# Kernel tuning notes

Measured on AMD Instinct MI355X. Metric: run time of the kernel, lower is better.

## Reference

```python
import jax, jax.numpy as jnp
import numpy as np

EMBED_DIM = 1024
HEAD_DIM = 64
B, T = 4, 4096


def setup_inputs() -> dict:
    key = jax.random.key(0)
    kx, kq, kk, kv = jax.random.split(key, 4)
    x = jax.random.normal(kx, (B, T, EMBED_DIM), dtype=jnp.float32)
    # nn.Linear weights, stored transposed as (in, out) for x @ W
    s = 1.0 / np.sqrt(EMBED_DIM)
    Wq = jax.random.normal(kq, (EMBED_DIM, HEAD_DIM), dtype=jnp.float32) * s
    Wk = jax.random.normal(kk, (EMBED_DIM, HEAD_DIM), dtype=jnp.float32) * s
    Wv = jax.random.normal(kv, (EMBED_DIM, HEAD_DIM), dtype=jnp.float32) * s
    return {"x": x, "Wq": Wq, "Wk": Wk, "Wv": Wv}


def reference(x, Wq, Wk, Wv):
    Bc, Tc, C = x.shape
    Q = x @ Wq  # [B, T, H]
    K = x @ Wk
    V = x @ Wv
    # NOTE: original scales by embedding_dim C, not head_dim
    scores = jnp.einsum('bqh,bkh->bqk', Q, K) / jnp.sqrt(jnp.float32(C))
    causal = jnp.tril(jnp.ones((Tc, Tc), dtype=bool))
    scores = jnp.where(causal, scores, -jnp.inf)
    attn = jax.nn.softmax(scores, axis=-1)
    return jnp.einsum('bqk,bkh->bqh', attn, V)
```

## Files before the change

kernel.cpp:

```cpp
#include <hip/hip_runtime.h>
#include <hip/hip_bf16.h>
#include <math.h>

typedef __attribute__((ext_vector_type(8))) short bf16x8;
typedef __attribute__((ext_vector_type(4))) float f32x4;

#define MFMA16 __builtin_amdgcn_mfma_f32_16x16x32_bf16

static constexpr int TSEQ = 4096;
static constexpr int EMB = 1024;
static constexpr int HD = 64;

__device__ __forceinline__ unsigned short f2bf(float f) {
    unsigned u = __builtin_bit_cast(unsigned, f);
    u += 0x7fffu + ((u >> 16) & 1u);
    return (unsigned short)(u >> 16);
}

__device__ __forceinline__ void gll16(const void* g, void* l) {
    __builtin_amdgcn_global_load_lds(
        (const __attribute__((address_space(1))) void*)g,
        (__attribute__((address_space(3))) void*)l, 16, 0, 0);
}

__global__ void prep_w(const float* __restrict__ Wq, const float* __restrict__ Wk,
                       const float* __restrict__ Wv, unsigned short* __restrict__ Wp) {
    int id = blockIdx.x * 256 + threadIdx.x;
    int wsel = id >> 16;
    int t = id & 65535;
    int k = t >> 6, n0 = t & 63;
    const float* W = (wsel == 0) ? Wq : (wsel == 1) ? Wk : Wv;
    float v = W[t];
    if (wsel == 0) v *= 0.03125f;
    int n = wsel * 64 + n0;
    Wp[(k >> 5) * 6144 + n * 32 + (k & 31)] = f2bf(v);
}

__global__ __launch_bounds__(512, 4) void proj_kernel(const float* __restrict__ X,
        const unsigned short* __restrict__ Wp, unsigned short* __restrict__ Qp,
        unsigned short* __restrict__ Kp, unsigned short* __restrict__ Vp) {
    __shared__ unsigned short wlds[2][6144];
    __shared__ unsigned short xlds[2][1024];

    const int tid = threadIdx.x;
    const int lane = tid & 63, wave = tid >> 6;
    const int col = lane & 15, quad = lane >> 4;
    const int mw = wave >> 2, nw = wave & 3;
    const int row0 = blockIdx.x * 32;

    f32x4 acc[3];
#pragma unroll
    for (int j = 0; j < 3; j++) acc[j] = (f32x4)(0.0f);

    const char* wsrc = (const char*)Wp + lane * 16;
    auto stageW = [&](int slab, int b) {
        const char* s = wsrc + (size_t)slab * 12288;
        char* d = (char*)&wlds[b][0];
        gll16(s + nw * 1024,       d + nw * 1024);
        gll16(s + (4 + nw) * 1024, d + (4 + nw) * 1024);
        gll16(s + (8 + nw) * 1024, d + (8 + nw) * 1024);
    };
    const int u = tid - 256;
    const int xrow = u >> 3, xseg = u & 7;
    const float* xsrc = X + (size_t)(row0 + xrow) * EMB + xseg * 4;
    const int xdst = (xrow >> 4) * 1024 + (xseg >> 1) * 256 + (xrow & 15) * 16 + (xseg & 1) * 8;

    float4 xg = (float4)(0.0f);
    if (mw == 1) {
        float4 v = *(const float4*)(xsrc);
        ushort4 p; p.x = f2bf(v.x); p.y = f2bf(v.y); p.z = f2bf(v.z); p.w = f2bf(v.w);
        *(ushort4*)((char*)&xlds[0][0] + xdst) = p;
        xg = *(const float4*)(xsrc + 32);
    } else {
        stageW(0, 0);
    }
    __syncthreads();

#pragma unroll 2
    for (int kc = 0; kc < 32; kc++) {
        const int b = kc & 1;
        if (mw == 0) {
            if (kc + 1 < 32) stageW(kc + 1, b ^ 1);
        } else {
            if (kc + 1 < 32) {
                float4 xn = xg;
                if (kc + 2 < 32) xn = *(const float4*)(xsrc + (kc + 2) * 32);
                ushort4 p; p.x = f2bf(xg.x); p.y = f2bf(xg.y);
                p.z = f2bf(xg.z); p.w = f2bf(xg.w);
                *(ushort4*)((char*)&xlds[b ^ 1][0] + xdst) = p;
                xg = xn;
            }
        }
        const bf16x8 A = *(const bf16x8*)((const char*)&xlds[b][0] + mw * 1024 + lane * 16);
        const char* wb = (const char*)&wlds[b][0] + col * 64 + quad * 16;
        acc[0] = MFMA16(A, *(const bf16x8*)(wb + nw * 1024),       acc[0], 0, 0, 0);
        acc[1] = MFMA16(A, *(const bf16x8*)(wb + (4 + nw) * 1024), acc[1], 0, 0, 0);
        acc[2] = MFMA16(A, *(const bf16x8*)(wb + (8 + nw) * 1024), acc[2], 0, 0, 0);
        __syncthreads();
    }

    const int tile = blockIdx.x * 2 + mw;
#pragma unroll
    for (int r = 0; r < 4; r++)
        Qp[tile * 1024 + (nw >> 1) * 512 + (quad * 4 + r) * 32 +
           ((nw & 1) * 2 + (col >> 3)) * 8 + (col & 7)] = f2bf(acc[0][r]);
#pragma unroll
    for (int r = 0; r < 4; r++)
        Kp[(tile * 2 + (nw >> 1)) * 512 + (quad * 4 + r) * 32 +
           ((nw & 1) * 2 + (col >> 3)) * 8 + (col & 7)] = f2bf(acc[1][r]);
    {
        ushort4 pk;
        pk.x = f2bf(acc[2][0]); pk.y = f2bf(acc[2][1]);
        pk.z = f2bf(acc[2][2]); pk.w = f2bf(acc[2][3]);
        *(ushort4*)&Vp[blockIdx.x * 2048 + nw * 512 + col * 32 + mw * 16 + quad * 4] = pk;
    }
}

__global__ __launch_bounds__(512, 4) void attn_kernel(const unsigned short* __restrict__ Qp,
        const unsigned short* __restrict__ Kp, const unsigned short* __restrict__ Vp,
        float* __restrict__ Out) {
    __shared__ float cmb[4][2][64][20];
    __shared__ unsigned short plds[8][2][640];
    const int lane = threadIdx.x & 63, wave = threadIdx.x >> 6;
    const int col = lane & 15, quad = lane >> 4;
    const int batch = blockIdx.x & 3;
    const int ti = 127 - (blockIdx.x >> 2);
    const int q0 = ti * 32;
    const size_t bT = (size_t)batch * TSEQ;
    const int fragoff = col * 64 + quad * 16;

    const char* QpB = (const char*)Qp;
    const char* KpB = (const char*)Kp;
    const char* VpB = (const char*)Vp;
    const int gt = (int)((bT + q0) >> 4);
    const int c0 = (int)(bT >> 5);

    bf16x8 aq[2][2];
#pragma unroll
    for (int m = 0; m < 2; m++)
#pragma unroll
        for (int h = 0; h < 2; h++)
            aq[m][h] = *(const bf16x8*)(QpB + (size_t)((gt + m) * 2 + h) * 1024 + fragoff);

    f32x4 o[2][4];
    f32x4 lsum[2];
#pragma unroll
    for (int m = 0; m < 2; m++) {
        lsum[m] = (f32x4)(0.0f);
#pragma unroll
        for (int t = 0; t < 4; t++) o[m][t] = (f32x4)(0.0f);
    }

    for (int c = wave; c <= ti; c += 8) {
        const char* kb = KpB + (size_t)(c0 + c) * 4096;
        const char* vb = VpB + (size_t)(c0 + c) * 4096;
        bf16x8 bk[2][2], bv[4];
#pragma unroll
        for (int j = 0; j < 2; j++)
#pragma unroll
            for (int h = 0; h < 2; h++)
                bk[j][h] = *(const bf16x8*)(kb + j * 2048 + h * 1024 + fragoff);
#pragma unroll
        for (int t = 0; t < 4; t++)
            bv[t] = *(const bf16x8*)(vb + t * 1024 + fragoff);

        f32x4 s[2][2];
#pragma unroll
        for (int m = 0; m < 2; m++)
#pragma unroll
            for (int j = 0; j < 2; j++) {
                f32x4 a = MFMA16(aq[m][0], bk[j][0], (f32x4)(0.0f), 0, 0, 0);
                s[m][j] = MFMA16(aq[m][1], bk[j][1], a, 0, 0, 0);
            }
        const bool diag = (c == ti);
#pragma unroll
        for (int m = 0; m < 2; m++)
#pragma unroll
            for (int j = 0; j < 2; j++)
#pragma unroll
                for (int r = 0; r < 4; r++) {
                    float v = s[m][j][r];
                    if (diag && (j * 16 + col > m * 16 + quad * 4 + r)) v = -INFINITY;
                    const float p = __expf(v);
                    lsum[m][r] += p;
                    plds[wave][m][(quad * 4 + r) * 40 + j * 16 + col] =
                        (unsigned short)(__builtin_bit_cast(unsigned, p) >> 16);
                }
        bf16x8 pa[2];
#pragma unroll
        for (int m = 0; m < 2; m++)
            pa[m] = *(const bf16x8*)(&plds[wave][m][col * 40 + quad * 8]);
#pragma unroll
        for (int m = 0; m < 2; m++)
#pragma unroll
            for (int t = 0; t < 4; t++)
                o[m][t] = MFMA16(pa[m], bv[t], o[m][t], 0, 0, 0);
    }

    auto wr = [&](int s) {
#pragma unroll
        for (int m = 0; m < 2; m++) {
#pragma unroll
            for (int t = 0; t < 4; t++)
                *(f32x4*)&cmb[s][m][lane][t * 4] = o[m][t];
            *(f32x4*)&cmb[s][m][lane][16] = lsum[m];
        }
    };
    auto rd = [&](int s) {
#pragma unroll
        for (int m = 0; m < 2; m++) {
#pragma unroll
            for (int t = 0; t < 4; t++)
                o[m][t] += *(const f32x4*)&cmb[s][m][lane][t * 4];
            lsum[m] += *(const f32x4*)&cmb[s][m][lane][16];
        }
    };
    if (wave >= 4) wr(wave - 4);
    __syncthreads();
    if (wave < 4) rd(wave);
    __syncthreads();
    if (wave == 2 || wave == 3) wr(wave);
    __syncthreads();
    if (wave < 2) rd(wave + 2);
    __syncthreads();
    if (wave == 1) wr(1);
    __syncthreads();
    if (wave == 0) {
        rd(1);
#pragma unroll
        for (int off = 1; off < 16; off <<= 1)
#pragma unroll
            for (int m = 0; m < 2; m++)
#pragma unroll
                for (int r = 0; r < 4; r++)
                    lsum[m][r] += __shfl_xor(lsum[m][r], off, 64);
#pragma unroll
        for (int m = 0; m < 2; m++)
#pragma unroll
            for (int r = 0; r < 4; r++) {
                const float inv = 1.0f / lsum[m][r];
                const size_t orow = (bT + q0 + m * 16 + quad * 4 + r) * HD;
#pragma unroll
                for (int t = 0; t < 4; t++)
                    Out[orow + t * 16 + col] = o[m][t][r] * inv;
            }
    }
}

extern "C" void kernel_launch(void* const* d_in, const int* in_sizes, int n_in,
                              void* d_out, int out_size, void* d_ws, size_t ws_size,
                              hipStream_t stream) {
    const float* x  = (const float*)d_in[0];
    const float* Wq = (const float*)d_in[1];
    const float* Wk = (const float*)d_in[2];
    const float* Wv = (const float*)d_in[3];
    float* out = (float*)d_out;

    char* w = (char*)d_ws;
    unsigned short* Wp = (unsigned short*)(w);
    unsigned short* Qp = (unsigned short*)(w + (512 << 10));
    unsigned short* Kp = (unsigned short*)(w + (512 << 10) + (2 << 20));
    unsigned short* Vp = (unsigned short*)(w + (512 << 10) + (4 << 20));

    hipLaunchKernelGGL(prep_w, dim3(768), dim3(256), 0, stream, Wq, Wk, Wv, Wp);
    hipLaunchKernelGGL(proj_kernel, dim3(512), dim3(512), 0, stream, x, Wp, Qp, Kp, Vp);
    hipLaunchKernelGGL(attn_kernel, dim3(512), dim3(512), 0, stream, Qp, Kp, Vp, out);
}
```

Before: 147.2 us.

## Enlarge projection tile to 64 rows and double K-step per stage

The projection kernel now handles 64 rows per block instead of 32, so each wave computes two M tiles and reuses each loaded weight fragment twice. Each pipeline stage stages two 32-wide K slabs, halving barrier count, and warp specialization now uses waves 0-3 for weight DMA and 4-7 for x conversion. The weight prep layout is changed to a fragment-contiguous order so LDS reads are linear per lane. The grid shrinks to 256 blocks with more LDS per block and occupancy is reduced to 2, which lowers parallelism.

After: 139.9 us. -4.9%, faster.

```diff
diff --git a/kernel.cpp b/kernel.cpp
--- a/kernel.cpp
+++ b/kernel.cpp
@@ -33,86 +33,141 @@
     float v = W[t];
     if (wsel == 0) v *= 0.03125f;
     int n = wsel * 64 + n0;
-    Wp[(k >> 5) * 6144 + n * 32 + (k & 31)] = f2bf(v);
-}
-
-__global__ __launch_bounds__(512, 4) void proj_kernel(const float* __restrict__ X,
+    Wp[(k >> 5) * 6144 + (n >> 4) * 512 + ((k >> 3) & 3) * 128 + (n & 15) * 8 + (k & 7)] = f2bf(v);
+}
+
+__global__ __launch_bounds__(512, 2) void proj_kernel(const float* __restrict__ X,
         const unsigned short* __restrict__ Wp, unsigned short* __restrict__ Qp,
         unsigned short* __restrict__ Kp, unsigned short* __restrict__ Vp) {
-    __shared__ unsigned short wlds[2][6144];
-    __shared__ unsigned short xlds[2][1024];
+    __shared__ unsigned short wlds[2][12288];
+    __shared__ unsigned short xlds[2][4096];
 
     const int tid = threadIdx.x;
     const int lane = tid & 63, wave = tid >> 6;
     const int col = lane & 15, quad = lane >> 4;
     const int mw = wave >> 2, nw = wave & 3;
-    const int row0 = blockIdx.x * 32;
-
-    f32x4 acc[3];
-#pragma unroll
-    for (int j = 0; j < 3; j++) acc[j] = (f32x4)(0.0f);
+    const int row0 = blockIdx.x * 64;
+
+    f32x4 acc[2][3];
+#pragma unroll
+    for (int i = 0; i < 2; i++)
+#pragma unroll
+        for (int j = 0; j < 3; j++) acc[i][j] = (f32x4)(0.0f);
 
     const char* wsrc = (const char*)Wp + lane * 16;
-    auto stageW = [&](int slab, int b) {
-        const char* s = wsrc + (size_t)slab * 12288;
-        char* d = (char*)&wlds[b][0];
-        gll16(s + nw * 1024,       d + nw * 1024);
-        gll16(s + (4 + nw) * 1024, d + (4 + nw) * 1024);
-        gll16(s + (8 + nw) * 1024, d + (8 + nw) * 1024);
-    };
-    const int u = tid - 256;
-    const int xrow = u >> 3, xseg = u & 7;
-    const float* xsrc = X + (size_t)(row0 + xrow) * EMB + xseg * 4;
-    const int xdst = (xrow >> 4) * 1024 + (xseg >> 1) * 256 + (xrow & 15) * 16 + (xseg & 1) * 8;
-
-    float4 xg = (float4)(0.0f);
-    if (mw == 1) {
-        float4 v = *(const float4*)(xsrc);
-        ushort4 p; p.x = f2bf(v.x); p.y = f2bf(v.y); p.z = f2bf(v.z); p.w = f2bf(v.w);
-        *(ushort4*)((char*)&xlds[0][0] + xdst) = p;
-        xg = *(const float4*)(xsrc + 32);
+    auto stageW = [&](int p, int b) {
+#pragma unroll
+        for (int u = 0; u < 2; u++) {
+            const char* s = wsrc + (size_t)(2 * p + u) * 12288;
+            char* d = (char*)&wlds[b][0] + u * 12288;
+            gll16(s + nw * 1024,       d + nw * 1024);
+            gll16(s + (4 + nw) * 1024, d + (4 + nw) * 1024);
+            gll16(s + (8 + nw) * 1024, d + (8 + nw) * 1024);
+        }
+    };
+    const int u2 = tid & 255;
+    const int xrow = u2 >> 3, q8 = u2 & 7;
+    const float* xsA = X + (size_t)(row0 + xrow) * EMB + q8 * 8;
+    const float* xsB = xsA + 32 * EMB;
+    const int xo = (q8 >> 2) * 4096 + (xrow >> 4) * 1024 + (q8 & 3) * 256 + (xrow & 15) * 16;
+
+    auto wr8 = [&](int b, int off, float4 f0, float4 f1) {
+        union { unsigned short s[8]; bf16x8 v; } r;
+        r.s[0] = f2bf(f0.x); r.s[1] = f2bf(f0.y); r.s[2] = f2bf(f0.z); r.s[3] = f2bf(f0.w);
+        r.s[4] = f2bf(f1.x); r.s[5] = f2bf(f1.y); r.s[6] = f2bf(f1.z); r.s[7] = f2bf(f1.w);
+        *(bf16x8*)((char*)&xlds[b][0] + off) = r.v;
+    };
+    auto compute = [&](int b) {
+        bf16x8 A[2][2], Wf[2][3];
+        const char* xb = (const char*)&xlds[b][0];
+        const char* wb = (const char*)&wlds[b][0];
+#pragma unroll
+        for (int u = 0; u < 2; u++) {
+#pragma unroll
+            for (int i = 0; i < 2; i++)
+                A[u][i] = *(const bf16x8*)(xb + u * 4096 + (mw * 2 + i) * 1024 + lane * 16);
+#pragma unroll
+            for (int j = 0; j < 3; j++)
+                Wf[u][j] = *(const bf16x8*)(wb + u * 12288 + (j * 4 + nw) * 1024 + lane * 16);
+        }
+#pragma unroll
+        for (int u = 0; u < 2; u++)
+#pragma unroll
+            for (int i = 0; i < 2; i++)
+#pragma unroll
+                for (int j = 0; j < 3; j++)
+                    acc[i][j] = MFMA16(A[u][i], Wf[u][j], acc[i][j], 0, 0, 0);
+    };
+
+    float4 pa0, pa1, pb0, pb1;
+    float4 qa0, qa1, qb0, qb1;
+    if (wave < 4) {
+        stageW(0, 0);
     } else {
-        stageW(0, 0);
-    }
-    __syncthreads();
-
-#pragma unroll 2
-    for (int kc = 0; kc < 32; kc++) {
-        const int b = kc & 1;
-        if (mw == 0) {
-            if (kc + 1 < 32) stageW(kc + 1, b ^ 1);
+        float4 t0 = *(const float4*)(xsA);
+        float4 t1 = *(const float4*)(xsA + 4);
+        float4 t2 = *(const float4*)(xsB);
+        float4 t3 = *(const float4*)(xsB + 4);
+        wr8(0, xo, t0, t1);
+        wr8(0, xo + 2048, t2, t3);
+        pa0 = *(const float4*)(xsA + 64);
+        pa1 = *(const float4*)(xsA + 68);
+        pb0 = *(const float4*)(xsB + 64);
+        pb1 = *(const float4*)(xsB + 68);
+    }
+    __syncthreads();
+
+    for (int kci = 0; kci < 8; kci++) {
+        const int kc0 = kci * 2;
+        if (wave >= 4) {
+            if (kc0 + 2 < 16) {
+                qa0 = *(const float4*)(xsA + (kc0 + 2) * 64);
+                qa1 = *(const float4*)(xsA + (kc0 + 2) * 64 + 4);
+                qb0 = *(const float4*)(xsB + (kc0 + 2) * 64);
+                qb1 = *(const float4*)(xsB + (kc0 + 2) * 64 + 4);
+            }
+            if (kc0 + 1 < 16) {
+                wr8(1, xo, pa0, pa1);
+                wr8(1, xo + 2048, pb0, pb1);
+            }
         } else {
-            if (kc + 1 < 32) {
-                float4 xn = xg;
-                if (kc + 2 < 32) xn = *(const float4*)(xsrc + (kc + 2) * 32);
-                ushort4 p; p.x = f2bf(xg.x); p.y = f2bf(xg.y);
-                p.z = f2bf(xg.z); p.w = f2bf(xg.w);
-                *(ushort4*)((char*)&xlds[b ^ 1][0] + xdst) = p;
-                xg = xn;
-            }
-        }
-        const bf16x8 A = *(const bf16x8*)((const char*)&xlds[b][0] + mw * 1024 + lane * 16);
-        const char* wb = (const char*)&wlds[b][0] + col * 64 + quad * 16;
-        acc[0] = MFMA16(A, *(const bf16x8*)(wb + nw * 1024),       acc[0], 0, 0, 0);
-        acc[1] = MFMA16(A, *(const bf16x8*)(wb + (4 + nw) * 1024), acc[1], 0, 0, 0);
-        acc[2] = MFMA16(A, *(const bf16x8*)(wb + (8 + nw) * 1024), acc[2], 0, 0, 0);
+            if (kc0 + 1 < 16) stageW(kc0 + 1, 1);
+        }
+        compute(0);
         __syncthreads();
-    }
-
-    const int tile = blockIdx.x * 2 + mw;
-#pragma unroll
-    for (int r = 0; r < 4; r++)
-        Qp[tile * 1024 + (nw >> 1) * 512 + (quad * 4 + r) * 32 +
-           ((nw & 1) * 2 + (col >> 3)) * 8 + (col & 7)] = f2bf(acc[0][r]);
-#pragma unroll
-    for (int r = 0; r < 4; r++)
-        Kp[(tile * 2 + (nw >> 1)) * 512 + (quad * 4 + r) * 32 +
-           ((nw & 1) * 2 + (col >> 3)) * 8 + (col & 7)] = f2bf(acc[1][r]);
-    {
+        if (wave >= 4) {
+            if (kc0 + 3 < 16) {
+                pa0 = *(const float4*)(xsA + (kc0 + 3) * 64);
+                pa1 = *(const float4*)(xsA + (kc0 + 3) * 64 + 4);
+                pb0 = *(const float4*)(xsB + (kc0 + 3) * 64);
+                pb1 = *(const float4*)(xsB + (kc0 + 3) * 64 + 4);
+            }
+            if (kc0 + 2 < 16) {
+                wr8(0, xo, qa0, qa1);
+                wr8(0, xo + 2048, qb0, qb1);
+            }
+        } else {
+            if (kc0 + 2 < 16) stageW(kc0 + 2, 0);
+        }
+        compute(1);
+        __syncthreads();
+    }
+
+#pragma unroll
+    for (int i = 0; i < 2; i++) {
+        const int t = blockIdx.x * 4 + mw * 2 + i;
+#pragma unroll
+        for (int r = 0; r < 4; r++)
+            Qp[t * 1024 + (nw >> 1) * 512 + (quad * 4 + r) * 32 +
+               ((nw & 1) * 2 + (col >> 3)) * 8 + (col & 7)] = f2bf(acc[i][0][r]);
+#pragma unroll
+        for (int r = 0; r < 4; r++)
+            Kp[(t * 2 + (nw >> 1)) * 512 + (quad * 4 + r) * 32 +
+               ((nw & 1) * 2 + (col >> 3)) * 8 + (col & 7)] = f2bf(acc[i][1][r]);
         ushort4 pk;
-        pk.x = f2bf(acc[2][0]); pk.y = f2bf(acc[2][1]);
-        pk.z = f2bf(acc[2][2]); pk.w = f2bf(acc[2][3]);
-        *(ushort4*)&Vp[blockIdx.x * 2048 + nw * 512 + col * 32 + mw * 16 + quad * 4] = pk;
+        pk.x = f2bf(acc[i][2][0]); pk.y = f2bf(acc[i][2][1]);
+        pk.z = f2bf(acc[i][2][2]); pk.w = f2bf(acc[i][2][3]);
+        *(ushort4*)&Vp[(t >> 1) * 2048 + nw * 512 + col * 32 + (t & 1) * 16 + quad * 4] = pk;
     }
 }
 
@@ -263,6 +318,6 @@
     unsigned short* Vp = (unsigned short*)(w + (512 << 10) + (4 << 20));
 
     hipLaunchKernelGGL(prep_w, dim3(768), dim3(256), 0, stream, Wq, Wk, Wv, Wp);
-    hipLaunchKernelGGL(proj_kernel, dim3(512), dim3(512), 0, stream, x, Wp, Qp, Kp, Vp);
+    hipLaunchKernelGGL(proj_kernel, dim3(256), dim3(512), 0, stream, x, Wp, Qp, Kp, Vp);
     hipLaunchKernelGGL(attn_kernel, dim3(512), dim3(512), 0, stream, Qp, Kp, Vp, out);
 }
```

## Double K-chunk per stage in projection kernel with MFMA-friendly weight layout

Applied to the files above, without the earlier changes.

The projection kernel now processes 64 K-elements per pipeline stage instead of 32, halving the number of barriers and loop iterations. Staging duties are split by wave: waves 0-3 load weights and waves 4-7 load and convert X, with 8-element vectorized LDS writes. The packed weight layout is reordered so each lane reads a contiguous 16-byte fragment, avoiding strided LDS reads. LDS usage doubles, which may reduce occupancy.

After: 138.4 us. 6.0% less time.

```diff
diff --git a/kernel.cpp b/kernel.cpp
--- a/kernel.cpp
+++ b/kernel.cpp
@@ -33,14 +33,14 @@
     float v = W[t];
     if (wsel == 0) v *= 0.03125f;
     int n = wsel * 64 + n0;
-    Wp[(k >> 5) * 6144 + n * 32 + (k & 31)] = f2bf(v);
+    Wp[(k >> 5) * 6144 + (n >> 4) * 512 + ((k >> 3) & 3) * 128 + (n & 15) * 8 + (k & 7)] = f2bf(v);
 }
 
 __global__ __launch_bounds__(512, 4) void proj_kernel(const float* __restrict__ X,
         const unsigned short* __restrict__ Wp, unsigned short* __restrict__ Qp,
         unsigned short* __restrict__ Kp, unsigned short* __restrict__ Vp) {
-    __shared__ unsigned short wlds[2][6144];
-    __shared__ unsigned short xlds[2][1024];
+    __shared__ unsigned short wlds[2][12288];
+    __shared__ unsigned short xlds[2][2048];
 
     const int tid = threadIdx.x;
     const int lane = tid & 63, wave = tid >> 6;
@@ -53,49 +53,80 @@
     for (int j = 0; j < 3; j++) acc[j] = (f32x4)(0.0f);
 
     const char* wsrc = (const char*)Wp + lane * 16;
-    auto stageW = [&](int slab, int b) {
-        const char* s = wsrc + (size_t)slab * 12288;
-        char* d = (char*)&wlds[b][0];
-        gll16(s + nw * 1024,       d + nw * 1024);
-        gll16(s + (4 + nw) * 1024, d + (4 + nw) * 1024);
-        gll16(s + (8 + nw) * 1024, d + (8 + nw) * 1024);
-    };
-    const int u = tid - 256;
-    const int xrow = u >> 3, xseg = u & 7;
-    const float* xsrc = X + (size_t)(row0 + xrow) * EMB + xseg * 4;
-    const int xdst = (xrow >> 4) * 1024 + (xseg >> 1) * 256 + (xrow & 15) * 16 + (xseg & 1) * 8;
-
-    float4 xg = (float4)(0.0f);
-    if (mw == 1) {
-        float4 v = *(const float4*)(xsrc);
-        ushort4 p; p.x = f2bf(v.x); p.y = f2bf(v.y); p.z = f2bf(v.z); p.w = f2bf(v.w);
-        *(ushort4*)((char*)&xlds[0][0] + xdst) = p;
-        xg = *(const float4*)(xsrc + 32);
+    auto stageW = [&](int p, int b) {
+#pragma unroll
+        for (int u = 0; u < 2; u++) {
+            const char* s = wsrc + (size_t)(2 * p + u) * 12288;
+            char* d = (char*)&wlds[b][0] + u * 12288;
+            gll16(s + nw * 1024,       d + nw * 1024);
+            gll16(s + (4 + nw) * 1024, d + (4 + nw) * 1024);
+            gll16(s + (8 + nw) * 1024, d + (8 + nw) * 1024);
+        }
+    };
+    const int u2 = tid & 255;
+    const int xrow = u2 >> 3, q8 = u2 & 7;
+    const float* xsrc = X + (size_t)(row0 + xrow) * EMB + q8 * 8;
+    const int xo = (q8 >> 2) * 2048 + (xrow >> 4) * 1024 + (q8 & 3) * 256 + (xrow & 15) * 16;
+
+    auto wr8 = [&](int b, float4 f0, float4 f1) {
+        union { unsigned short s[8]; bf16x8 v; } r;
+        r.s[0] = f2bf(f0.x); r.s[1] = f2bf(f0.y); r.s[2] = f2bf(f0.z); r.s[3] = f2bf(f0.w);
+        r.s[4] = f2bf(f1.x); r.s[5] = f2bf(f1.y); r.s[6] = f2bf(f1.z); r.s[7] = f2bf(f1.w);
+        *(bf16x8*)((char*)&xlds[b][0] + xo) = r.v;
+    };
+    auto compute = [&](int b) {
+        bf16x8 A[2], Wf[2][3];
+        const char* xb = (const char*)&xlds[b][0];
+        const char* wb = (const char*)&wlds[b][0];
+#pragma unroll
+        for (int u = 0; u < 2; u++) {
+            A[u] = *(const bf16x8*)(xb + u * 2048 + mw * 1024 + lane * 16);
+#pragma unroll
+            for (int j = 0; j < 3; j++)
+                Wf[u][j] = *(const bf16x8*)(wb + u * 12288 + (j * 4 + nw) * 1024 + lane * 16);
+        }
+#pragma unroll
+        for (int u = 0; u < 2; u++)
+#pragma unroll
+            for (int j = 0; j < 3; j++)
+                acc[j] = MFMA16(A[u], Wf[u][j], acc[j], 0, 0, 0);
+    };
+
+    float4 pa0, pa1, qa0, qa1;
+    if (wave < 4) {
+        stageW(0, 0);
     } else {
-        stageW(0, 0);
-    }
-    __syncthreads();
-
-#pragma unroll 2
-    for (int kc = 0; kc < 32; kc++) {
-        const int b = kc & 1;
-        if (mw == 0) {
-            if (kc + 1 < 32) stageW(kc + 1, b ^ 1);
+        float4 t0 = *(const float4*)(xsrc);
+        float4 t1 = *(const float4*)(xsrc + 4);
+        wr8(0, t0, t1);
+        pa0 = *(const float4*)(xsrc + 64);
+        pa1 = *(const float4*)(xsrc + 68);
+    }
+    __syncthreads();
+
+    for (int kci = 0; kci < 8; kci++) {
+        const int s0 = kci * 2;
+        if (wave >= 4) {
+            if (s0 + 2 < 16) {
+                qa0 = *(const float4*)(xsrc + (s0 + 2) * 64);
+                qa1 = *(const float4*)(xsrc + (s0 + 2) * 64 + 4);
+            }
+            if (s0 + 1 < 16) wr8(1, pa0, pa1);
         } else {
-            if (kc + 1 < 32) {
-                float4 xn = xg;
-                if (kc + 2 < 32) xn = *(const float4*)(xsrc + (kc + 2) * 32);
-                ushort4 p; p.x = f2bf(xg.x); p.y = f2bf(xg.y);
-                p.z = f2bf(xg.z); p.w = f2bf(xg.w);
-                *(ushort4*)((char*)&xlds[b ^ 1][0] + xdst) = p;
-                xg = xn;
-            }
-        }
-        const bf16x8 A = *(const bf16x8*)((const char*)&xlds[b][0] + mw * 1024 + lane * 16);
-        const char* wb = (const char*)&wlds[b][0] + col * 64 + quad * 16;
-        acc[0] = MFMA16(A, *(const bf16x8*)(wb + nw * 1024),       acc[0], 0, 0, 0);
-        acc[1] = MFMA16(A, *(const bf16x8*)(wb + (4 + nw) * 1024), acc[1], 0, 0, 0);
-        acc[2] = MFMA16(A, *(const bf16x8*)(wb + (8 + nw) * 1024), acc[2], 0, 0, 0);
+            if (s0 + 1 < 16) stageW(s0 + 1, 1);
+        }
+        compute(0);
+        __syncthreads();
+        if (wave >= 4) {
+            if (s0 + 3 < 16) {
+                pa0 = *(const float4*)(xsrc + (s0 + 3) * 64);
+                pa1 = *(const float4*)(xsrc + (s0 + 3) * 64 + 4);
+            }
+            if (s0 + 2 < 16) wr8(0, qa0, qa1);
+        } else {
+            if (s0 + 2 < 16) stageW(s0 + 2, 0);
+        }
+        compute(1);
         __syncthreads();
     }
 
```
